# Performance work log

Hardware: AMD Instinct MI355X
Metric: run time of the kernel (lower is better)

Reference implementation:

```python
import jax, jax.numpy as jnp
import numpy as np

N_NODES = 100000
IN_CH = 256
OUT_CH = 128
N_EDGES = 3200000
SCALING_FACTOR = 1.8


def gcn_propagate(x, edge_index, num_nodes):
    """APPNP(K=1, alpha=0) == one step of D^-1/2 (A+I) D^-1/2 @ x."""
    row, col = edge_index[0], edge_index[1]
    loops = jnp.arange(num_nodes, dtype=edge_index.dtype)
    row = jnp.concatenate([row, loops])
    col = jnp.concatenate([col, loops])
    ones = jnp.ones(row.shape[0], dtype=x.dtype)
    deg = jax.ops.segment_sum(ones, col, num_segments=num_nodes)  # [N]
    dinv = jnp.where(deg > 0, jax.lax.rsqrt(deg), 0.0)
    norm = dinv[row] * dinv[col]  # [E+N]
    msgs = x[row] * norm[:, None]  # gather + scale, [E+N, C]
    return jax.ops.segment_sum(msgs, col, num_segments=num_nodes)  # [N, C]


def setup_inputs() -> dict:
    key = jax.random.key(0)
    ks = jax.random.split(key, 7)
    x = jax.random.normal(ks[0], (N_NODES, IN_CH), dtype=jnp.float32)
    edge_index = jax.random.randint(ks[1], (2, N_EDGES), 0, N_NODES, dtype=jnp.int64)
    s1 = 1.0 / np.sqrt(IN_CH)
    W1 = jax.random.uniform(ks[2], (IN_CH, OUT_CH), jnp.float32, -s1, s1)
    b1 = jax.random.uniform(ks[3], (OUT_CH,), jnp.float32, -s1, s1)
    W2 = jax.random.uniform(ks[4], (IN_CH, OUT_CH), jnp.float32, -s1, s1)
    b2 = jax.random.uniform(ks[5], (OUT_CH,), jnp.float32, -s1, s1)
    return {"x": x, "edge_index": edge_index, "W1": W1, "b1": b1, "W2": W2, "b2": b2}


def reference(x, edge_index, W1, b1, W2, b2):
    num_nodes = x.shape[0]
    # branch 1: linear1 then propagate
    x_ = x @ W1 + b1
    x_ = gcn_propagate(x_, edge_index, num_nodes)
    # branch 2: linear2, L2 normalize per-row, scale, then propagate
    h = x @ W2 + b2
    nrm = jnp.sqrt(jnp.sum(h * h, axis=1, keepdims=True))
    h = h / jnp.maximum(nrm, 1e-12) * SCALING_FACTOR
    h = gcn_propagate(h, edge_index, num_nodes)
    return (h, x_)
```

## Files before the change

### kernel.cpp

```cpp
#include <hip/hip_runtime.h>

#define IN_CH   256
#define OUT_CH  128
#define SCALE   1.8f
#define GT_M    32
#define BKT_SH  8
#define BKT_CAP 9216

using bf16x8 = __attribute__((ext_vector_type(8))) short;
using f32x4  = __attribute__((ext_vector_type(4))) float;

__device__ __forceinline__ float blo(unsigned int w) { return __uint_as_float(w << 16); }
__device__ __forceinline__ float bhi(unsigned int w) { return __uint_as_float(w & 0xffff0000u); }
__device__ __forceinline__ unsigned short f2b(float f) {
    unsigned int u = __float_as_uint(f);
    u += 0x7fffu + ((u >> 16) & 1u);
    return (unsigned short)(u >> 16);
}
__device__ __forceinline__ void split2(float f, unsigned short& h, unsigned short& l) {
    h = f2b(f);
    float hf = __uint_as_float((unsigned int)h << 16);
    l = f2b(f - hf);
}

__global__ void init_kernel(int* __restrict__ bktCur) {
    int i = blockIdx.x * blockDim.x + threadIdx.x;
    if (i < 512) bktCur[i] = i * BKT_CAP;
}

__global__ __launch_bounds__(256) void part_kernel(const int* __restrict__ row, const int* __restrict__ col,
                                                   int* __restrict__ bktCur, unsigned int* __restrict__ pairs,
                                                   int E, int NBKT) {
    __shared__ int lh[512];
    __shared__ int lcur[512];
    int t = threadIdx.x;
    lh[t] = 0; lh[t + 256] = 0;
    __syncthreads();
    int tile = (E + gridDim.x - 1) / gridDim.x;
    int e0 = blockIdx.x * tile;
    int e1 = min(E, e0 + tile);
    for (int i = e0 + t; i < e1; i += 256)
        atomicAdd(&lh[col[i] >> BKT_SH], 1);
    __syncthreads();
    for (int b = t; b < 512; b += 256) {
        int c = (b < NBKT) ? lh[b] : 0;
        lcur[b] = (c > 0) ? atomicAdd(&bktCur[b], c) : 0;
    }
    __syncthreads();
    for (int i = e0 + t; i < e1; i += 256) {
        int c = col[i];
        int b = c >> BKT_SH;
        int pos = atomicAdd(&lcur[b], 1);
        pairs[pos] = ((unsigned int)(c & 255) << 17) | (unsigned int)row[i];
    }
}

__global__ __launch_bounds__(256) void csr_kernel(const unsigned int* __restrict__ pairs,
                                                  const int* __restrict__ bktCur,
                                                  int* __restrict__ csr, int* __restrict__ offs,
                                                  int* __restrict__ deg, float* __restrict__ dinv,
                                                  int N) {
    __shared__ unsigned int sorted[BKT_CAP];
    __shared__ int sh[512];
    __shared__ int sc[512];
    __shared__ int s[256];
    __shared__ int nc[256];
    __shared__ int ncur[256];
    int b = blockIdx.x;
    int t = threadIdx.x;
    int base = b * BKT_CAP;
    int cnt = bktCur[b] - base;

    sh[t] = 0; sh[t + 256] = 0;
    __syncthreads();
    for (int i = t; i < cnt; i += 256)
        atomicAdd(&sh[(pairs[base + i] & 0x1FFFF) >> 8], 1);
    __syncthreads();

    int v0 = sh[t];
    s[t] = v0;
    __syncthreads();
    for (int o = 1; o < 256; o <<= 1) {
        int u = (t >= o) ? s[t - o] : 0;
        __syncthreads();
        s[t] += u;
        __syncthreads();
    }
    sc[t] = s[t] - v0;
    int tot0 = s[255];
    __syncthreads();
    int v1 = sh[t + 256];
    s[t] = v1;
    __syncthreads();
    for (int o = 1; o < 256; o <<= 1) {
        int u = (t >= o) ? s[t - o] : 0;
        __syncthreads();
        s[t] += u;
        __syncthreads();
    }
    sc[t + 256] = s[t] - v1 + tot0;
    __syncthreads();

    for (int i = t; i < cnt; i += 256) {
        unsigned int k = pairs[base + i];
        int pos = atomicAdd(&sc[(k & 0x1FFFF) >> 8], 1);
        sorted[pos] = k;
    }
    __syncthreads();

    nc[t] = 0;
    __syncthreads();
    for (int i = t; i < cnt; i += 256)
        atomicAdd(&nc[sorted[i] >> 17], 1);
    __syncthreads();
    int dv = nc[t];
    s[t] = dv;
    __syncthreads();
    for (int o = 1; o < 256; o <<= 1) {
        int u = (t >= o) ? s[t - o] : 0;
        __syncthreads();
        s[t] += u;
        __syncthreads();
    }
    int rel = s[t] - dv;
    int n = (b << BKT_SH) + t;
    if (n < N) {
        offs[n] = base + rel;
        deg[n] = dv;
        dinv[n] = 1.0f / sqrtf((float)dv + 1.0f);
    }
    ncur[t] = rel;
    __syncthreads();
    for (int i = t; i < cnt; i += 256) {
        unsigned int k = sorted[i];
        int node = k >> 17;
        int pos = atomicAdd(&ncur[node], 1);
        csr[base + pos] = (int)(k & 0x1FFFF);
    }
}

__global__ __launch_bounds__(256) void wsplit_kernel(const float* __restrict__ W1, const float* __restrict__ b1,
                                                     const float* __restrict__ W2, const float* __restrict__ b2,
                                                     unsigned short* __restrict__ Wht, unsigned short* __restrict__ Wlt,
                                                     float* __restrict__ bc) {
    int n = blockIdx.x;
    int k = threadIdx.x;
    float w = (n < OUT_CH) ? W2[k * OUT_CH + n] : W1[k * OUT_CH + (n - OUT_CH)];
    unsigned short h, l;
    split2(w, h, l);
    Wht[n * IN_CH + k] = h;
    Wlt[n * IN_CH + k] = l;
    if (k == 0) bc[n] = (n < OUT_CH) ? b2[n] : b1[n - OUT_CH];
}

#define XPAD 264
__global__ __launch_bounds__(256) void gemm_mfma_kernel(const float* __restrict__ x,
                                                        const unsigned short* __restrict__ Wht,
                                                        const unsigned short* __restrict__ Wlt,
                                                        const float* __restrict__ bc,
                                                        const float* __restrict__ dinv,
                                                        unsigned short* __restrict__ gb) {
    __shared__ unsigned short xh[GT_M * XPAD];
    __shared__ unsigned short xl[GT_M * XPAD];
    __shared__ float sn[2 * GT_M];

    int t = threadIdx.x;
    size_t row0 = (size_t)blockIdx.x * GT_M;

    const float4* xg = (const float4*)(x + row0 * IN_CH);
#pragma unroll
    for (int i = 0; i < 8; i++) {
        int f4 = t + i * 256;
        float4 v = xg[f4];
        int row = f4 >> 6;
        int c4 = (f4 & 63) * 4;
        unsigned short h0, h1, h2, h3, l0, l1, l2, l3;
        split2(v.x, h0, l0); split2(v.y, h1, l1);
        split2(v.z, h2, l2); split2(v.w, h3, l3);
        uint2 hw, lw;
        hw.x = (unsigned int)h0 | ((unsigned int)h1 << 16);
        hw.y = (unsigned int)h2 | ((unsigned int)h3 << 16);
        lw.x = (unsigned int)l0 | ((unsigned int)l1 << 16);
        lw.y = (unsigned int)l2 | ((unsigned int)l3 << 16);
        *(uint2*)&xh[row * XPAD + c4] = hw;
        *(uint2*)&xl[row * XPAD + c4] = lw;
    }
    __syncthreads();

    int lane = t & 63;
    int wv = t >> 6;
    int lr = lane & 15;
    int lk = (lane >> 4) * 8;

    f32x4 acc[2][4];
#pragma unroll
    for (int rt = 0; rt < 2; rt++)
#pragma unroll
        for (int ct = 0; ct < 4; ct++) acc[rt][ct] = (f32x4){0.f, 0.f, 0.f, 0.f};

#pragma unroll
    for (int kt = 0; kt < 8; kt++) {
        int k0 = kt * 32;
        bf16x8 ah[2], al[2];
#pragma unroll
        for (int rt = 0; rt < 2; rt++) {
            int idx = (rt * 16 + lr) * XPAD + k0 + lk;
            ah[rt] = *(const bf16x8*)&xh[idx];
            al[rt] = *(const bf16x8*)&xl[idx];
        }
        bf16x8 bh[4], bl[4];
#pragma unroll
        for (int ct = 0; ct < 4; ct++) {
            int n = wv * 64 + ct * 16 + lr;
            bh[ct] = *(const bf16x8*)&Wht[n * IN_CH + k0 + lk];
            bl[ct] = *(const bf16x8*)&Wlt[n * IN_CH + k0 + lk];
        }
#pragma unroll
        for (int rt = 0; rt < 2; rt++)
#pragma unroll
            for (int ct = 0; ct < 4; ct++) {
                acc[rt][ct] = __builtin_amdgcn_mfma_f32_16x16x32_bf16(ah[rt], bh[ct], acc[rt][ct], 0, 0, 0);
                acc[rt][ct] = __builtin_amdgcn_mfma_f32_16x16x32_bf16(al[rt], bh[ct], acc[rt][ct], 0, 0, 0);
                acc[rt][ct] = __builtin_amdgcn_mfma_f32_16x16x32_bf16(ah[rt], bl[ct], acc[rt][ct], 0, 0, 0);
            }
    }
    __syncthreads();

    float bcv[4];
#pragma unroll
    for (int ct = 0; ct < 4; ct++) bcv[ct] = bc[wv * 64 + ct * 16 + lr];
#pragma unroll
    for (int rt = 0; rt < 2; rt++)
#pragma unroll
        for (int ct = 0; ct < 4; ct++)
#pragma unroll
            for (int j = 0; j < 4; j++) acc[rt][ct][j] += bcv[ct];

    if (wv < 2) {
        float nr[2][4];
#pragma unroll
        for (int rt = 0; rt < 2; rt++)
#pragma unroll
            for (int j = 0; j < 4; j++) {
                float sum = 0.f;
#pragma unroll
                for (int ct = 0; ct < 4; ct++) sum += acc[rt][ct][j] * acc[rt][ct][j];
                nr[rt][j] = sum;
            }
#pragma unroll
        for (int o = 1; o < 16; o <<= 1)
#pragma unroll
            for (int rt = 0; rt < 2; rt++)
#pragma unroll
                for (int j = 0; j < 4; j++) nr[rt][j] += __shfl_xor(nr[rt][j], o);
        if (lr == 0) {
#pragma unroll
            for (int rt = 0; rt < 2; rt++)
#pragma unroll
                for (int j = 0; j < 4; j++)
                    sn[wv * GT_M + rt * 16 + (lane >> 4) * 4 + j] = nr[rt][j];
        }
    }
    __syncthreads();

#pragma unroll
    for (int rt = 0; rt < 2; rt++) {
#pragma unroll
        for (int j = 0; j < 4; j++) {
            int rl = rt * 16 + (lane >> 4) * 4 + j;
            float dn = dinv[row0 + rl];
            float sf;
            if (wv < 2) {
                float n2 = sn[rl] + sn[GT_M + rl];
                sf = SCALE * dn / fmaxf(sqrtf(n2), 1e-12f);
            } else {
                sf = dn;
            }
            size_t base = (row0 + rl) * 256;
#pragma unroll
            for (int ct = 0; ct < 4; ct++) {
                int col = wv * 64 + ct * 16 + lr;
                gb[base + col] = f2b(acc[rt][ct][j] * sf);
            }
        }
    }
}

__global__ __launch_bounds__(256) void gather_kernel(const uint4* __restrict__ gp,
                                                     const int* __restrict__ offs, const int* __restrict__ deg,
                                                     const int* __restrict__ csr, const float* __restrict__ dinv,
                                                     float* __restrict__ outh, float* __restrict__ outx, int N) {
    int t = threadIdx.x;
    int n = (blockIdx.x << 2) + (t >> 6);
    if (n >= N) return;
    int l = t & 63;
    int half = l >> 5;
    int cl = l & 31;

    float a0 = 0.f, a1 = 0.f, a2 = 0.f, a3 = 0.f, a4 = 0.f, a5 = 0.f, a6 = 0.f, a7 = 0.f;
    auto accum = [&](uint4 w) {
        a0 += blo(w.x); a1 += bhi(w.x);
        a2 += blo(w.y); a3 += bhi(w.y);
        a4 += blo(w.z); a5 += bhi(w.z);
        a6 += blo(w.w); a7 += bhi(w.w);
    };

    if (half == 0) accum(gp[(size_t)n * 32 + cl]);

    int s0 = offs[n];
    int e1 = s0 + deg[n];
    int e = s0 + half;
    for (; e + 2 < e1; e += 4) {
        int sa = csr[e];
        int sb = csr[e + 2];
        uint4 wa = gp[(size_t)sa * 32 + cl];
        uint4 wb = gp[(size_t)sb * 32 + cl];
        accum(wa); accum(wb);
    }
    for (; e < e1; e += 2) {
        accum(gp[(size_t)csr[e] * 32 + cl]);
    }

    a0 += __shfl_xor(a0, 32);
    a1 += __shfl_xor(a1, 32);
    a2 += __shfl_xor(a2, 32);
    a3 += __shfl_xor(a3, 32);
    a4 += __shfl_xor(a4, 32);
    a5 += __shfl_xor(a5, 32);
    a6 += __shfl_xor(a6, 32);
    a7 += __shfl_xor(a7, 32);

    if (half == 0) {
        float dn = dinv[n];
        float4 v0 = {a0 * dn, a1 * dn, a2 * dn, a3 * dn};
        float4 v1 = {a4 * dn, a5 * dn, a6 * dn, a7 * dn};
        if (cl < 16) {
            float* o = &outh[(size_t)n * OUT_CH + cl * 8];
            *(float4*)o = v0;
            *(float4*)(o + 4) = v1;
        } else {
            float* o = &outx[(size_t)n * OUT_CH + (cl - 16) * 8];
            *(float4*)o = v0;
            *(float4*)(o + 4) = v1;
        }
    }
}

extern "C" void kernel_launch(void* const* d_in, const int* in_sizes, int n_in,
                              void* d_out, int out_size, void* d_ws, size_t ws_size,
                              hipStream_t stream) {
    const float* x   = (const float*)d_in[0];
    const int*   ei  = (const int*)d_in[1];
    const float* W1  = (const float*)d_in[2];
    const float* b1  = (const float*)d_in[3];
    const float* W2  = (const float*)d_in[4];
    const float* b2  = (const float*)d_in[5];

    const int N = in_sizes[0] / IN_CH;
    const int E = in_sizes[1] / 2;
    const int NBKT = (N + 255) >> BKT_SH;

    float* outh = (float*)d_out;
    float* outx = outh + (size_t)N * OUT_CH;

    char* p = (char*)d_ws;
    auto take = [&](size_t bytes) {
        char* q = p;
        p += (bytes + 255) & ~(size_t)255;
        return q;
    };
    int*   deg     = (int*)take((size_t)N * sizeof(int));
    float* dinv    = (float*)take((size_t)N * sizeof(float));
    int*   offs    = (int*)take((size_t)N * sizeof(int));
    int*   bktCur  = (int*)take(512 * sizeof(int));
    float* bc      = (float*)take(256 * sizeof(float));
    unsigned short* Wht = (unsigned short*)take(256 * 256 * sizeof(unsigned short));
    unsigned short* Wlt = (unsigned short*)take(256 * 256 * sizeof(unsigned short));
    int*   csr     = (int*)take((size_t)NBKT * BKT_CAP * sizeof(int));
    unsigned short* gb = (unsigned short*)take((size_t)N * 256 * sizeof(unsigned short));
    unsigned int* pairs = (unsigned int*)gb;

    const int* erow = ei;
    const int* ecol = ei + E;

    init_kernel<<<2, 256, 0, stream>>>(bktCur);
    wsplit_kernel<<<256, 256, 0, stream>>>(W1, b1, W2, b2, Wht, Wlt, bc);
    part_kernel<<<512, 256, 0, stream>>>(erow, ecol, bktCur, pairs, E, NBKT);
    csr_kernel<<<NBKT, 256, 0, stream>>>(pairs, bktCur, csr, offs, deg, dinv, N);

    gemm_mfma_kernel<<<N / GT_M, 256, 0, stream>>>(x, Wht, Wlt, bc, dinv, gb);

    gather_kernel<<<(N + 3) / 4, 256, 0, stream>>>((const uint4*)gb, offs, deg, csr, dinv, outh, outx, N);
}
```

Before: 451.1 us.

## Overlap graph partition/CSR build with GEMM via fused heterogeneous kernels

The GEMM no longer needs dinv. Source-side normalization moves into the gather, which now reads dinv[src] per edge, so the GEMM no longer depends on the CSR build. GEMM blocks are split in half and co-scheduled with the partition and CSR kernels in two merged launches, letting the independent work overlap. The init kernel is folded into wsplit, and pairs gets its own workspace buffer instead of aliasing gb. The cost is an extra random dinv load per edge in the gather, larger shared memory in the merged kernels that may lower occupancy for GEMM blocks, and more workspace.

New measurement: 435.7 us. -3.4%, faster.

```diff
diff --git a/kernel.cpp b/kernel.cpp
--- a/kernel.cpp
+++ b/kernel.cpp
@@ -23,21 +23,34 @@
     l = f2b(f - hf);
 }
 
-__global__ void init_kernel(int* __restrict__ bktCur) {
-    int i = blockIdx.x * blockDim.x + threadIdx.x;
-    if (i < 512) bktCur[i] = i * BKT_CAP;
-}
-
-__global__ __launch_bounds__(256) void part_kernel(const int* __restrict__ row, const int* __restrict__ col,
-                                                   int* __restrict__ bktCur, unsigned int* __restrict__ pairs,
-                                                   int E, int NBKT) {
-    __shared__ int lh[512];
-    __shared__ int lcur[512];
+__global__ __launch_bounds__(256) void wsplit_kernel(const float* __restrict__ W1, const float* __restrict__ b1,
+                                                     const float* __restrict__ W2, const float* __restrict__ b2,
+                                                     unsigned short* __restrict__ Wht, unsigned short* __restrict__ Wlt,
+                                                     float* __restrict__ bc, int* __restrict__ bktCur) {
+    int n = blockIdx.x;
+    int k = threadIdx.x;
+    if (n < 2) {
+        int i = n * 256 + k;
+        bktCur[i] = i * BKT_CAP;
+    }
+    float w = (n < OUT_CH) ? W2[k * OUT_CH + n] : W1[k * OUT_CH + (n - OUT_CH)];
+    unsigned short h, l;
+    split2(w, h, l);
+    Wht[n * IN_CH + k] = h;
+    Wlt[n * IN_CH + k] = l;
+    if (k == 0) bc[n] = (n < OUT_CH) ? b2[n] : b1[n - OUT_CH];
+}
+
+__device__ __forceinline__ void part_body(char* smem, const int* __restrict__ row, const int* __restrict__ col,
+                                          int* __restrict__ bktCur, unsigned int* __restrict__ pairs,
+                                          int E, int NBKT, int nPart, int pb) {
+    int* lh   = (int*)smem;
+    int* lcur = lh + 512;
     int t = threadIdx.x;
     lh[t] = 0; lh[t + 256] = 0;
     __syncthreads();
-    int tile = (E + gridDim.x - 1) / gridDim.x;
-    int e0 = blockIdx.x * tile;
+    int tile = (E + nPart - 1) / nPart;
+    int e0 = pb * tile;
     int e1 = min(E, e0 + tile);
     for (int i = e0 + t; i < e1; i += 256)
         atomicAdd(&lh[col[i] >> BKT_SH], 1);
@@ -55,18 +68,17 @@
     }
 }
 
-__global__ __launch_bounds__(256) void csr_kernel(const unsigned int* __restrict__ pairs,
-                                                  const int* __restrict__ bktCur,
-                                                  int* __restrict__ csr, int* __restrict__ offs,
-                                                  int* __restrict__ deg, float* __restrict__ dinv,
-                                                  int N) {
-    __shared__ unsigned int sorted[BKT_CAP];
-    __shared__ int sh[512];
-    __shared__ int sc[512];
-    __shared__ int s[256];
-    __shared__ int nc[256];
-    __shared__ int ncur[256];
-    int b = blockIdx.x;
+__device__ __forceinline__ void csr_body(char* smem, const unsigned int* __restrict__ pairs,
+                                         const int* __restrict__ bktCur,
+                                         int* __restrict__ csr, int* __restrict__ offs,
+                                         int* __restrict__ deg, float* __restrict__ dinv,
+                                         int N, int b) {
+    unsigned int* sorted = (unsigned int*)smem;
+    int* sh   = (int*)(smem + 36864);
+    int* sc   = (int*)(smem + 38912);
+    int* s    = (int*)(smem + 40960);
+    int* nc   = (int*)(smem + 41984);
+    int* ncur = (int*)(smem + 43008);
     int t = threadIdx.x;
     int base = b * BKT_CAP;
     int cnt = bktCur[b] - base;
@@ -139,33 +151,18 @@
     }
 }
 
-__global__ __launch_bounds__(256) void wsplit_kernel(const float* __restrict__ W1, const float* __restrict__ b1,
-                                                     const float* __restrict__ W2, const float* __restrict__ b2,
-                                                     unsigned short* __restrict__ Wht, unsigned short* __restrict__ Wlt,
-                                                     float* __restrict__ bc) {
-    int n = blockIdx.x;
-    int k = threadIdx.x;
-    float w = (n < OUT_CH) ? W2[k * OUT_CH + n] : W1[k * OUT_CH + (n - OUT_CH)];
-    unsigned short h, l;
-    split2(w, h, l);
-    Wht[n * IN_CH + k] = h;
-    Wlt[n * IN_CH + k] = l;
-    if (k == 0) bc[n] = (n < OUT_CH) ? b2[n] : b1[n - OUT_CH];
-}
-
 #define XPAD 264
-__global__ __launch_bounds__(256) void gemm_mfma_kernel(const float* __restrict__ x,
-                                                        const unsigned short* __restrict__ Wht,
-                                                        const unsigned short* __restrict__ Wlt,
-                                                        const float* __restrict__ bc,
-                                                        const float* __restrict__ dinv,
-                                                        unsigned short* __restrict__ gb) {
-    __shared__ unsigned short xh[GT_M * XPAD];
-    __shared__ unsigned short xl[GT_M * XPAD];
-    __shared__ float sn[2 * GT_M];
+__device__ __forceinline__ void gemm_body(char* smem, const float* __restrict__ x,
+                                          const unsigned short* __restrict__ Wht,
+                                          const unsigned short* __restrict__ Wlt,
+                                          const float* __restrict__ bc,
+                                          unsigned short* __restrict__ gb, int blockRow) {
+    unsigned short* xh = (unsigned short*)smem;
+    unsigned short* xl = xh + GT_M * XPAD;
+    float* sn = (float*)(smem + 2 * GT_M * XPAD * sizeof(unsigned short));
 
     int t = threadIdx.x;
-    size_t row0 = (size_t)blockIdx.x * GT_M;
+    size_t row0 = (size_t)blockRow * GT_M;
 
     const float4* xg = (const float4*)(x + row0 * IN_CH);
 #pragma unroll
@@ -268,13 +265,12 @@
 #pragma unroll
         for (int j = 0; j < 4; j++) {
             int rl = rt * 16 + (lane >> 4) * 4 + j;
-            float dn = dinv[row0 + rl];
             float sf;
             if (wv < 2) {
                 float n2 = sn[rl] + sn[GT_M + rl];
-                sf = SCALE * dn / fmaxf(sqrtf(n2), 1e-12f);
+                sf = SCALE / fmaxf(sqrtf(n2), 1e-12f);
             } else {
-                sf = dn;
+                sf = 1.0f;
             }
             size_t base = (row0 + rl) * 256;
 #pragma unroll
@@ -284,6 +280,36 @@
             }
         }
     }
+}
+
+__global__ __launch_bounds__(256) void k1_part_gemm(const int* __restrict__ row, const int* __restrict__ col,
+                                                    int* __restrict__ bktCur, unsigned int* __restrict__ pairs,
+                                                    int E, int NBKT, int nPart,
+                                                    const float* __restrict__ x,
+                                                    const unsigned short* __restrict__ Wht,
+                                                    const unsigned short* __restrict__ Wlt,
+                                                    const float* __restrict__ bc,
+                                                    unsigned short* __restrict__ gb) {
+    __shared__ __align__(16) char smem[34048];
+    int b = (int)blockIdx.x;
+    if (b < nPart) part_body(smem, row, col, bktCur, pairs, E, NBKT, nPart, b);
+    else gemm_body(smem, x, Wht, Wlt, bc, gb, b - nPart);
+}
+
+__global__ __launch_bounds__(256) void k2_csr_gemm(const unsigned int* __restrict__ pairs,
+                                                   const int* __restrict__ bktCur,
+                                                   int* __restrict__ csr, int* __restrict__ offs,
+                                                   int* __restrict__ deg, float* __restrict__ dinv,
+                                                   int N, int nCsr, int gemmRowBase,
+                                                   const float* __restrict__ x,
+                                                   const unsigned short* __restrict__ Wht,
+                                                   const unsigned short* __restrict__ Wlt,
+                                                   const float* __restrict__ bc,
+                                                   unsigned short* __restrict__ gb) {
+    __shared__ __align__(16) char smem[44032];
+    int b = (int)blockIdx.x;
+    if (b < nCsr) csr_body(smem, pairs, bktCur, csr, offs, deg, dinv, N, b);
+    else gemm_body(smem, x, Wht, Wlt, bc, gb, gemmRowBase + (b - nCsr));
 }
 
 __global__ __launch_bounds__(256) void gather_kernel(const uint4* __restrict__ gp,
@@ -298,14 +324,15 @@
     int cl = l & 31;
 
     float a0 = 0.f, a1 = 0.f, a2 = 0.f, a3 = 0.f, a4 = 0.f, a5 = 0.f, a6 = 0.f, a7 = 0.f;
-    auto accum = [&](uint4 w) {
-        a0 += blo(w.x); a1 += bhi(w.x);
-        a2 += blo(w.y); a3 += bhi(w.y);
-        a4 += blo(w.z); a5 += bhi(w.z);
-        a6 += blo(w.w); a7 += bhi(w.w);
+    auto accumw = [&](uint4 w, float ds) {
+        a0 += blo(w.x) * ds; a1 += bhi(w.x) * ds;
+        a2 += blo(w.y) * ds; a3 += bhi(w.y) * ds;
+        a4 += blo(w.z) * ds; a5 += bhi(w.z) * ds;
+        a6 += blo(w.w) * ds; a7 += bhi(w.w) * ds;
     };
 
-    if (half == 0) accum(gp[(size_t)n * 32 + cl]);
+    float dn = dinv[n];
+    if (half == 0) accumw(gp[(size_t)n * 32 + cl], dn);
 
     int s0 = offs[n];
     int e1 = s0 + deg[n];
@@ -313,12 +340,15 @@
     for (; e + 2 < e1; e += 4) {
         int sa = csr[e];
         int sb = csr[e + 2];
+        float da = dinv[sa];
+        float db = dinv[sb];
         uint4 wa = gp[(size_t)sa * 32 + cl];
         uint4 wb = gp[(size_t)sb * 32 + cl];
-        accum(wa); accum(wb);
+        accumw(wa, da); accumw(wb, db);
     }
     for (; e < e1; e += 2) {
-        accum(gp[(size_t)csr[e] * 32 + cl]);
+        int sa = csr[e];
+        accumw(gp[(size_t)sa * 32 + cl], dinv[sa]);
     }
 
     a0 += __shfl_xor(a0, 32);
@@ -331,7 +361,6 @@
     a7 += __shfl_xor(a7, 32);
 
     if (half == 0) {
-        float dn = dinv[n];
         float4 v0 = {a0 * dn, a1 * dn, a2 * dn, a3 * dn};
         float4 v1 = {a4 * dn, a5 * dn, a6 * dn, a7 * dn};
         if (cl < 16) {
@@ -377,18 +406,21 @@
     unsigned short* Wht = (unsigned short*)take(256 * 256 * sizeof(unsigned short));
     unsigned short* Wlt = (unsigned short*)take(256 * 256 * sizeof(unsigned short));
     int*   csr     = (int*)take((size_t)NBKT * BKT_CAP * sizeof(int));
+    unsigned int* pairs = (unsigned int*)take((size_t)NBKT * BKT_CAP * sizeof(unsigned int));
     unsigned short* gb = (unsigned short*)take((size_t)N * 256 * sizeof(unsigned short));
-    unsigned int* pairs = (unsigned int*)gb;
 
     const int* erow = ei;
     const int* ecol = ei + E;
 
-    init_kernel<<<2, 256, 0, stream>>>(bktCur);
-    wsplit_kernel<<<256, 256, 0, stream>>>(W1, b1, W2, b2, Wht, Wlt, bc);
-    part_kernel<<<512, 256, 0, stream>>>(erow, ecol, bktCur, pairs, E, NBKT);
-    csr_kernel<<<NBKT, 256, 0, stream>>>(pairs, bktCur, csr, offs, deg, dinv, N);
-
-    gemm_mfma_kernel<<<N / GT_M, 256, 0, stream>>>(x, Wht, Wlt, bc, dinv, gb);
-
+    const int nPart = 512;
+    const int gemmBlocks = N / GT_M;
+    const int gemmA = (gemmBlocks + 1) / 2;
+    const int gemmB = gemmBlocks - gemmA;
+
+    wsplit_kernel<<<256, 256, 0, stream>>>(W1, b1, W2, b2, Wht, Wlt, bc, bktCur);
+    k1_part_gemm<<<nPart + gemmA, 256, 0, stream>>>(erow, ecol, bktCur, pairs, E, NBKT, nPart,
+                                                    x, Wht, Wlt, bc, gb);
+    k2_csr_gemm<<<NBKT + gemmB, 256, 0, stream>>>(pairs, bktCur, csr, offs, deg, dinv, N, NBKT, gemmA,
+                                                  x, Wht, Wlt, bc, gb);
     gather_kernel<<<(N + 3) / 4, 256, 0, stream>>>((const uint4*)gb, offs, deg, csr, dinv, outh, outx, N);
 }
```
